# Performance work log

Hardware: AMD Instinct MI355X
Metric: run time of the kernel (lower is better)

Reference implementation:

```python
import jax, jax.numpy as jnp
import numpy as np

NB_OBJ = 16
BATCH = 64
F_IN = 32768
HID = 64
N_AGENTS = 4
N_ACT = 13
NEG_SLOPE = 0.01  # torch LeakyReLU default


def _build_edges():
    # fully connected minus diagonal, per graph; GCNConv adds self-loops
    adj = np.ones((NB_OBJ, NB_OBJ)) - np.eye(NB_OBJ)
    r, c = np.nonzero(adj)
    loop = np.arange(NB_OBJ)
    src = np.concatenate([r, loop])
    dst = np.concatenate([c, loop])
    offs = (np.arange(BATCH) * NB_OBJ)[:, None]
    src_all = (src[None, :] + offs).reshape(-1)
    dst_all = (dst[None, :] + offs).reshape(-1)
    return jnp.asarray(src_all, jnp.int32), jnp.asarray(dst_all, jnp.int32)


def setup_inputs() -> dict:
    key = jax.random.key(0)
    ks = jax.random.split(key, 9)
    s = 1.0 / np.sqrt(F_IN)
    sh = 1.0 / np.sqrt(HID)
    return {
        "unary_tensor": jax.random.normal(ks[0], (BATCH, NB_OBJ, F_IN), jnp.float32),
        "binary_tensor": jax.random.uniform(ks[1], (BATCH, NB_OBJ, NB_OBJ, 2), jnp.float32),
        "actions": jax.random.normal(ks[2], (N_AGENTS, BATCH, N_ACT), jnp.float32),
        "gcn_w": jax.random.uniform(ks[3], (F_IN, HID), jnp.float32, -s, s),
        "gcn_b": jax.random.uniform(ks[4], (HID,), jnp.float32, -s, s),
        "head_w1": jax.random.uniform(ks[5], (N_AGENTS, HID, HID), jnp.float32, -sh, sh),
        "head_b1": jax.random.uniform(ks[6], (N_AGENTS, HID), jnp.float32, -sh, sh),
        "head_w2": jax.random.uniform(ks[7], (N_AGENTS, HID, N_ACT), jnp.float32, -sh, sh),
        "head_b2": jax.random.uniform(ks[8], (N_AGENTS, N_ACT), jnp.float32, -sh, sh),
    }


def reference(unary_tensor, binary_tensor, actions, gcn_w, gcn_b,
              head_w1, head_b1, head_w2, head_b2):
    src, dst = _build_edges()
    x = unary_tensor.reshape(BATCH * NB_OBJ, F_IN)  # flatten(0,1)
    lin = x @ gcn_w  # [1024, HID]
    # GCN symmetric norm: every node has degree 16 (15 neighbors + self loop)
    norm = 1.0 / NB_OBJ
    msg = lin[src] * norm
    agg = jax.ops.segment_sum(msg, dst, num_segments=BATCH * NB_OBJ)
    h = agg + gcn_b  # [1024, HID]
    # split into graphs and max-pool over nodes
    pooled = jnp.max(h.reshape(BATCH, NB_OBJ, HID), axis=1)  # [64, HID]
    # per-agent critic heads
    z = jnp.einsum('bh,ahk->abk', pooled, head_w1) + head_b1[:, None, :]
    z = jnp.where(z >= 0, z, NEG_SLOPE * z)  # LeakyReLU
    all_q = jnp.einsum('abh,ahk->abk', z, head_w2) + head_b2[:, None, :]  # [A,64,13]
    int_acs = jnp.argmax(actions, axis=2)  # [A, 64]
    q = jnp.take_along_axis(all_q, int_acs[:, :, None], axis=2)  # [A, 64, 1]
    return q
```

## Files before the change

kernel.cpp:

```cpp
#include <hip/hip_runtime.h>

#define F_IN    32768
#define HID     64
#define NB_OBJ  16
#define BATCH   64
#define N_AGENTS 4
#define N_ACT   13
#define NEG_SLOPE 0.01f

#define FC      64
#define NCHUNK  (F_IN / FC)

typedef float f32x4 __attribute__((ext_vector_type(4)));

__device__ float g_part[NCHUNK * BATCH * HID];
__device__ float g_part2[4 * BATCH * HID];

__global__ __launch_bounds__(512, 4)
void k_gcn_partial(const float* __restrict__ u, const float* __restrict__ w) {
    __shared__ float xbar[BATCH][FC + 4];
    const int t    = threadIdx.x;
    const int blk  = blockIdx.x;
    const int f0   = blk * FC;
    const int lane = t & 63;
    const int wv   = t >> 6;

    float wreg[FC];
    {
        const float* wp = w + (size_t)f0 * HID + lane;
        #pragma unroll
        for (int f = 0; f < FC; ++f) wreg[f] = wp[f * HID];
    }

    {
        const int b = t >> 3;
        const int j = t & 7;
        const float* up = u + (size_t)b * (NB_OBJ * F_IN) + f0 + j * 4;
        f32x4 a0 = (f32x4)(0.f);
        f32x4 a1 = (f32x4)(0.f);
        #pragma unroll
        for (int o = 0; o < NB_OBJ; ++o) {
            const float* ro = up + o * F_IN;
            f32x4 v0 = __builtin_nontemporal_load(reinterpret_cast<const f32x4*>(ro));
            f32x4 v1 = __builtin_nontemporal_load(reinterpret_cast<const f32x4*>(ro + 32));
            a0 += v0;
            a1 += v1;
        }
        const float inv = 1.0f / (float)NB_OBJ;
        a0 *= inv;
        a1 *= inv;
        *reinterpret_cast<f32x4*>(&xbar[b][j * 4])      = a0;
        *reinterpret_cast<f32x4*>(&xbar[b][32 + j * 4]) = a1;
    }
    __syncthreads();

    {
        float* pout = g_part + (size_t)blk * (BATCH * HID) + lane;
        #pragma unroll
        for (int bb = 0; bb < 8; ++bb) {
            const int b = wv * 8 + bb;
            float acc = 0.f;
            #pragma unroll
            for (int fq = 0; fq < FC / 4; ++fq) {
                f32x4 xb = *reinterpret_cast<const f32x4*>(&xbar[b][fq * 4]);
                acc += xb.x * wreg[fq * 4 + 0];
                acc += xb.y * wreg[fq * 4 + 1];
                acc += xb.z * wreg[fq * 4 + 2];
                acc += xb.w * wreg[fq * 4 + 3];
            }
            pout[b * HID] = acc;
        }
    }
}

__global__ __launch_bounds__(256)
void k_reduce() {
    __shared__ float red[4][HID];
    const int bid = blockIdx.x;
    const int q   = bid >> 6;
    const int b   = bid & 63;
    const int t   = threadIdx.x;
    const int h   = t & 63;
    const int kg  = t >> 6;

    const float* p = g_part + ((size_t)(q * 128 + kg * 32)) * (BATCH * HID)
                   + (size_t)b * HID + h;
    float acc = 0.f;
    #pragma unroll 8
    for (int i = 0; i < 32; ++i)
        acc += p[(size_t)i * (BATCH * HID)];
    red[kg][h] = acc;
    __syncthreads();

    if (t < HID)
        g_part2[((size_t)q * BATCH + b) * HID + t] =
            red[0][t] + red[1][t] + red[2][t] + red[3][t];
}

__global__ __launch_bounds__(256)
void k_heads(const float* __restrict__ gcn_b,
             const float* __restrict__ w1, const float* __restrict__ b1,
             const float* __restrict__ w2, const float* __restrict__ b2,
             const float* __restrict__ actions, float* __restrict__ out) {
    const int b = blockIdx.x;
    const int t = threadIdx.x;
    __shared__ float pooled[HID];
    __shared__ float zbuf[N_AGENTS][HID];
    __shared__ float qbuf[N_AGENTS][N_ACT];

    if (t < HID) {
        float acc = gcn_b[t];
        #pragma unroll
        for (int q = 0; q < 4; ++q)
            acc += g_part2[((size_t)q * BATCH + b) * HID + t];
        pooled[t] = acc;
    }
    __syncthreads();

    {
        const int a = t >> 6, k = t & 63;
        const float* w1p = w1 + a * (HID * HID) + k;
        float acc = b1[a * HID + k];
        #pragma unroll
        for (int hh = 0; hh < HID; ++hh) acc += pooled[hh] * w1p[hh * HID];
        zbuf[a][k] = (acc >= 0.f) ? acc : NEG_SLOPE * acc;
    }
    __syncthreads();

    if (t < N_AGENTS * N_ACT) {
        const int a = t / N_ACT, c = t % N_ACT;
        const float* w2p = w2 + a * (HID * N_ACT) + c;
        float acc = b2[a * N_ACT + c];
        #pragma unroll
        for (int hh = 0; hh < HID; ++hh) acc += zbuf[a][hh] * w2p[hh * N_ACT];
        qbuf[a][c] = acc;
    }
    __syncthreads();

    if (t < N_AGENTS) {
        const float* ap = actions + ((size_t)t * BATCH + b) * N_ACT;
        int best = 0; float bv = ap[0];
        for (int c = 1; c < N_ACT; ++c) {
            float v = ap[c];
            if (v > bv) { bv = v; best = c; }
        }
        out[t * BATCH + b] = qbuf[t][best];
    }
}

extern "C" void kernel_launch(void* const* d_in, const int* in_sizes, int n_in,
                              void* d_out, int out_size, void* d_ws, size_t ws_size,
                              hipStream_t stream) {
    const float* u   = (const float*)d_in[0];
    const float* act = (const float*)d_in[2];
    const float* gw  = (const float*)d_in[3];
    const float* gb  = (const float*)d_in[4];
    const float* w1  = (const float*)d_in[5];
    const float* b1  = (const float*)d_in[6];
    const float* w2  = (const float*)d_in[7];
    const float* b2  = (const float*)d_in[8];
    float* out = (float*)d_out;

    hipLaunchKernelGGL(k_gcn_partial, dim3(NCHUNK), dim3(512), 0, stream, u, gw);
    hipLaunchKernelGGL(k_reduce,      dim3(256),    dim3(256), 0, stream);
    hipLaunchKernelGGL(k_heads,       dim3(BATCH),  dim3(256), 0, stream,
                       gb, w1, b1, w2, b2, act, out);
}
```

Measured before the change: 39.49 us.

## Split GCN partial blocks by batch half and fuse reduction into heads kernel

The partial-product kernel now launches twice as many 256-thread blocks, each handling half the batch for a feature chunk, to raise parallelism. The separate reduce kernel and its intermediate buffer are removed; the heads kernel now sums all chunk partials itself with 512 threads per batch row. This saves a launch and a global round trip, but the final reduction runs on only 64 blocks and weight loads are duplicated across batch halves.

```diff
diff --git a/kernel.cpp b/kernel.cpp
--- a/kernel.cpp
+++ b/kernel.cpp
@@ -10,20 +10,22 @@
 
 #define FC      64
 #define NCHUNK  (F_IN / FC)
+#define BH      32
 
 typedef float f32x4 __attribute__((ext_vector_type(4)));
 
 __device__ float g_part[NCHUNK * BATCH * HID];
-__device__ float g_part2[4 * BATCH * HID];
 
-__global__ __launch_bounds__(512, 4)
+__global__ __launch_bounds__(256, 4)
 void k_gcn_partial(const float* __restrict__ u, const float* __restrict__ w) {
-    __shared__ float xbar[BATCH][FC + 4];
-    const int t    = threadIdx.x;
-    const int blk  = blockIdx.x;
-    const int f0   = blk * FC;
-    const int lane = t & 63;
-    const int wv   = t >> 6;
+    __shared__ float xbar[BH][FC + 4];
+    const int t     = threadIdx.x;
+    const int blk   = blockIdx.x >> 1;
+    const int bhalf = blockIdx.x & 1;
+    const int f0    = blk * FC;
+    const int b0    = bhalf * BH;
+    const int lane  = t & 63;
+    const int wv    = t >> 6;
 
     float wreg[FC];
     {
@@ -35,7 +37,7 @@
     {
         const int b = t >> 3;
         const int j = t & 7;
-        const float* up = u + (size_t)b * (NB_OBJ * F_IN) + f0 + j * 4;
+        const float* up = u + (size_t)(b0 + b) * (NB_OBJ * F_IN) + f0 + j * 4;
         f32x4 a0 = (f32x4)(0.f);
         f32x4 a1 = (f32x4)(0.f);
         #pragma unroll
@@ -55,7 +57,7 @@
     __syncthreads();
 
     {
-        float* pout = g_part + (size_t)blk * (BATCH * HID) + lane;
+        float* pout = g_part + (size_t)blk * (BATCH * HID) + (size_t)b0 * HID + lane;
         #pragma unroll
         for (int bb = 0; bb < 8; ++bb) {
             const int b = wv * 8 + bb;
@@ -73,51 +75,39 @@
     }
 }
 
-__global__ __launch_bounds__(256)
-void k_reduce() {
-    __shared__ float red[4][HID];
-    const int bid = blockIdx.x;
-    const int q   = bid >> 6;
-    const int b   = bid & 63;
-    const int t   = threadIdx.x;
-    const int h   = t & 63;
-    const int kg  = t >> 6;
-
-    const float* p = g_part + ((size_t)(q * 128 + kg * 32)) * (BATCH * HID)
-                   + (size_t)b * HID + h;
-    float acc = 0.f;
-    #pragma unroll 8
-    for (int i = 0; i < 32; ++i)
-        acc += p[(size_t)i * (BATCH * HID)];
-    red[kg][h] = acc;
-    __syncthreads();
-
-    if (t < HID)
-        g_part2[((size_t)q * BATCH + b) * HID + t] =
-            red[0][t] + red[1][t] + red[2][t] + red[3][t];
-}
-
-__global__ __launch_bounds__(256)
-void k_heads(const float* __restrict__ gcn_b,
-             const float* __restrict__ w1, const float* __restrict__ b1,
-             const float* __restrict__ w2, const float* __restrict__ b2,
-             const float* __restrict__ actions, float* __restrict__ out) {
+__global__ __launch_bounds__(512)
+void k_tail(const float* __restrict__ gcn_b,
+            const float* __restrict__ w1, const float* __restrict__ b1,
+            const float* __restrict__ w2, const float* __restrict__ b2,
+            const float* __restrict__ actions, float* __restrict__ out) {
     const int b = blockIdx.x;
     const int t = threadIdx.x;
+    __shared__ float red[8][HID];
     __shared__ float pooled[HID];
     __shared__ float zbuf[N_AGENTS][HID];
     __shared__ float qbuf[N_AGENTS][N_ACT];
 
+    {
+        const int h  = t & 63;
+        const int kg = t >> 6;
+        const float* p = g_part + (size_t)(kg * 64) * (BATCH * HID)
+                       + (size_t)b * HID + h;
+        float acc = 0.f;
+        #pragma unroll 16
+        for (int i = 0; i < 64; ++i)
+            acc += p[(size_t)i * (BATCH * HID)];
+        red[kg][h] = acc;
+    }
+    __syncthreads();
     if (t < HID) {
         float acc = gcn_b[t];
         #pragma unroll
-        for (int q = 0; q < 4; ++q)
-            acc += g_part2[((size_t)q * BATCH + b) * HID + t];
+        for (int kg = 0; kg < 8; ++kg) acc += red[kg][t];
         pooled[t] = acc;
     }
     __syncthreads();
 
-    {
+    if (t < N_AGENTS * HID) {
         const int a = t >> 6, k = t & 63;
         const float* w1p = w1 + a * (HID * HID) + k;
         float acc = b1[a * HID + k];
@@ -161,8 +151,7 @@
     const float* b2  = (const float*)d_in[8];
     float* out = (float*)d_out;
 
-    hipLaunchKernelGGL(k_gcn_partial, dim3(NCHUNK), dim3(512), 0, stream, u, gw);
-    hipLaunchKernelGGL(k_reduce,      dim3(256),    dim3(256), 0, stream);
-    hipLaunchKernelGGL(k_heads,       dim3(BATCH),  dim3(256), 0, stream,
+    hipLaunchKernelGGL(k_gcn_partial, dim3(NCHUNK * 2), dim3(256), 0, stream, u, gw);
+    hipLaunchKernelGGL(k_tail,        dim3(BATCH),      dim3(512), 0, stream,
                        gb, w1, b1, w2, b2, act, out);
 }
```

New measurement: 40.32 us. 1.02x slower.
